# Performance work log

Measured on AMD Instinct MI355X. Metric: run time of the kernel, lower is better.

Reference implementation:

```python
import jax, jax.numpy as jnp
import numpy as np

N_EMBD = 1024
N_HEAD = 16
HEAD_DIM = N_EMBD // N_HEAD


def setup_inputs() -> dict:
    key = jax.random.key(0)
    kx, kq, kk, kv, kp = jax.random.split(key, 5)
    B, S = 4, 2048
    x = jax.random.normal(kx, (B, S, N_EMBD), dtype=jnp.float32)
    # nn.Linear(n, n, bias=False): weight [out, in], y = x @ W.T
    s = 1.0 / np.sqrt(N_EMBD)
    Wq = jax.random.uniform(kq, (N_EMBD, N_EMBD), jnp.float32, -s, s)
    Wk = jax.random.uniform(kk, (N_EMBD, N_EMBD), jnp.float32, -s, s)
    Wv = jax.random.uniform(kv, (N_EMBD, N_EMBD), jnp.float32, -s, s)
    Wo = jax.random.uniform(kp, (N_EMBD, N_EMBD), jnp.float32, -s, s)
    return {"x": x, "Wq": Wq, "Wk": Wk, "Wv": Wv, "Wo": Wo}


def _split_heads(t):
    B, S, _ = t.shape
    return t.reshape(B, S, N_HEAD, HEAD_DIM).transpose(0, 2, 1, 3)  # [B,H,S,D]


def reference(x, Wq, Wk, Wv, Wo):
    q = _split_heads(x @ Wq.T)
    k = _split_heads(x @ Wk.T)
    v = _split_heads(x @ Wv.T)
    scale = 1.0 / np.sqrt(HEAD_DIM)
    scores = jnp.einsum('bhqd,bhkd->bhqk', q, k) * scale  # [B,H,S,S]
    S = x.shape[1]
    mask = jnp.tril(jnp.ones((S, S), dtype=bool))
    masked = jnp.where(mask[None, None], scores, -jnp.inf)
    attn = jax.nn.softmax(masked, axis=-1)
    heads = jnp.einsum('bhqk,bhkd->bhqd', attn, v)
    merged = heads.transpose(0, 2, 1, 3).reshape(x.shape[0], S, N_EMBD)
    return merged @ Wo.T
```

## Files before the change

kernel.cpp:

```cpp
#include <hip/hip_runtime.h>
#include <hip/hip_bf16.h>

typedef __hip_bfloat16 bf16;
typedef __attribute__((ext_vector_type(8))) short short8;
typedef __attribute__((ext_vector_type(4))) short short4v;
typedef __attribute__((ext_vector_type(4))) float f32x4;
typedef unsigned int uint32;

#define MFMA16(a, b, c) __builtin_amdgcn_mfma_f32_16x16x32_bf16(a, b, c, 0, 0, 0)

__device__ __forceinline__ f32x4 MFMA16K16(short4v a, short4v b, f32x4 c) {
#if __has_builtin(__builtin_amdgcn_mfma_f32_16x16x16bf16_1k)
    return __builtin_amdgcn_mfma_f32_16x16x16bf16_1k(a, b, c, 0, 0, 0);
#else
    asm("v_mfma_f32_16x16x16_bf16 %0, %1, %2, %0" : "+v"(c) : "v"(a), "v"(b));
    return c;
#endif
}

constexpr int EMB   = 1024;
constexpr int SEQ   = 2048;
constexpr int BATCH = 4;
constexpr int NH    = 16;
constexpr int HD    = 64;
constexpr int QKVW  = 3 * EMB;
constexpr float QSCALE = 0.125f * 1.44269504f;

__device__ __forceinline__ void gl_lds16(const bf16* g, bf16* l) {
    __builtin_amdgcn_global_load_lds(
        (const __attribute__((address_space(1))) void*)g,
        (__attribute__((address_space(3))) void*)l,
        16, 0, 0);
}

__device__ __forceinline__ float fexp2(float x) {
#if __has_builtin(__builtin_amdgcn_exp2f)
    return __builtin_amdgcn_exp2f(x);
#else
    return exp2f(x);
#endif
}

__device__ __forceinline__ uint32 pack2(float a, float b) {
    uint32 ua = __builtin_bit_cast(uint32, a) + 0x8000u;
    uint32 ub = __builtin_bit_cast(uint32, b) + 0x8000u;
    return __builtin_amdgcn_perm(ub, ua, 0x07060302u);
}

__device__ __forceinline__ bf16 fbf16(float f) {
    unsigned short u =
        (unsigned short)((__builtin_bit_cast(uint32, f) + 0x8000u) >> 16);
    return __builtin_bit_cast(bf16, u);
}

__global__ void convert_all(const float* __restrict__ x,
                            const float* __restrict__ wq,
                            const float* __restrict__ wk,
                            const float* __restrict__ wv,
                            const float* __restrict__ wo,
                            bf16* __restrict__ xc,
                            bf16* __restrict__ wqkv,
                            bf16* __restrict__ woc) {
    const int NX = BATCH * SEQ * EMB;
    const int NW = EMB * EMB;
    const float* src; bf16* dst; int n4, b0, nb;
    const int blk = blockIdx.x;
    if (blk < 2048)      { src = x;  dst = xc;          n4 = NX / 4; b0 = 0;    nb = 2048; }
    else if (blk < 2304) { src = wq; dst = wqkv;        n4 = NW / 4; b0 = 2048; nb = 256; }
    else if (blk < 2560) { src = wk; dst = wqkv + NW;   n4 = NW / 4; b0 = 2304; nb = 256; }
    else if (blk < 2816) { src = wv; dst = wqkv + 2*NW; n4 = NW / 4; b0 = 2560; nb = 256; }
    else                 { src = wo; dst = woc;         n4 = NW / 4; b0 = 2816; nb = 256; }
    for (int i = (blk - b0) * 256 + threadIdx.x; i < n4; i += nb * 256) {
        float4 v = ((const float4*)src)[i];
        uint2 o;
        o.x = pack2(v.x, v.y);
        o.y = pack2(v.z, v.w);
        ((uint2*)dst)[i] = o;
    }
}

template <typename OutT>
__global__ __launch_bounds__(256) void gemm_bt(const bf16* __restrict__ A,
                                               const bf16* __restrict__ B,
                                               OutT* __restrict__ C,
                                               int M, int N, int K,
                                               float oscale, int qlim) {
    __shared__ __align__(16) bf16 As[2][128 * 64];
    __shared__ __align__(16) bf16 Bs[2][128 * 64];

    const int t    = threadIdx.x;
    const int lane = t & 63;
    const int wid  = t >> 6;
    const int l16  = lane & 15;
    const int quad = lane >> 4;
    const int e    = l16 & 7;
    const int wm   = (wid >> 1) * 64;
    const int wn   = (wid & 1) * 64;

    const int nwg   = (int)gridDim.x;
    const int cpx   = nwg >> 3;
    const int gx    = N >> 7;
    const int mrows = cpx / gx;
    const int xcd   = (int)blockIdx.x & 7;
    const int local = (int)blockIdx.x >> 3;
    const int m0    = (xcd * mrows + (local % mrows)) * 128;
    const int n0    = (local / mrows) * 128;
    const float sc  = (n0 < qlim) ? oscale : 1.0f;

    f32x4 acc[4][4] = {};
    const int srow = lane >> 3;
    const int scol = ((lane & 7) ^ srow) * 8;

    auto stage = [&](int kt, int buf) {
        const int k0 = kt * 64;
        #pragma unroll
        for (int it = 0; it < 4; ++it) {
            int rb = it * 32 + wid * 8;
            gl_lds16(&A[(size_t)(m0 + rb + srow) * K + k0 + scol], &As[buf][rb * 64]);
            gl_lds16(&B[(size_t)(n0 + rb + srow) * K + k0 + scol], &Bs[buf][rb * 64]);
        }
    };

    const int nk = K >> 6;
    stage(0, 0);
    stage(1, 1);

    for (int kt = 0; kt < nk; ++kt) {
        const int cur = kt & 1;
        if (kt < nk - 1) __builtin_amdgcn_s_waitcnt(0x0F78);
        else             __builtin_amdgcn_s_waitcnt(0x0F70);
        __builtin_amdgcn_s_barrier();

        #pragma unroll
        for (int ks = 0; ks < 64; ks += 32) {
            const int cb = (ks >> 3) + quad;
            short8 af[4], bfr[4];
            #pragma unroll
            for (int i = 0; i < 4; ++i)
                af[i] = *(const short8*)&As[cur][(wm + i * 16 + l16) * 64 + ((cb ^ e) * 8)];
            #pragma unroll
            for (int j = 0; j < 4; ++j)
                bfr[j] = *(const short8*)&Bs[cur][(wn + j * 16 + l16) * 64 + ((cb ^ e) * 8)];
            #pragma unroll
            for (int i = 0; i < 4; ++i)
                #pragma unroll
                for (int j = 0; j < 4; ++j)
                    acc[i][j] = MFMA16(af[i], bfr[j], acc[i][j]);
        }

        __builtin_amdgcn_s_barrier();
        if (kt + 2 < nk) stage(kt + 2, cur);
    }

    #pragma unroll
    for (int i = 0; i < 4; ++i)
        #pragma unroll
        for (int j = 0; j < 4; ++j)
            #pragma unroll
            for (int r = 0; r < 4; ++r) {
                int row = m0 + wm + i * 16 + quad * 4 + r;
                int col = n0 + wn + j * 16 + l16;
                float v = acc[i][j][r] * sc;
                if constexpr (sizeof(OutT) == 2)
                    C[(size_t)row * N + col] = fbf16(v);
                else
                    C[(size_t)row * N + col] = (OutT)v;
            }
}

__global__ __launch_bounds__(256) void transpose_v(const bf16* __restrict__ QKV,
                                                   bf16* __restrict__ Vt) {
    __shared__ __align__(16) bf16 Ts[4096];
    const int t  = threadIdx.x;
    const int st = blockIdx.x;
    const int bh = blockIdx.y;
    const int b  = bh >> 4, h = bh & 15;
    const int s0 = st * 64;

    const bf16* src = QKV + ((size_t)(b * SEQ + s0)) * QKVW + 2 * EMB + h * HD;
    {
        int r = t >> 3, cq = t & 7;
        #pragma unroll
        for (int it = 0; it < 2; ++it, r += 32) {
            uint4 v = *(const uint4*)&src[(size_t)r * QKVW + cq * 8];
            int blk = cq ^ (r >> 3);
            *(uint4*)&Ts[r * 64 + blk * 8] = v;
        }
    }
    __syncthreads();
    bf16* dst = Vt + (size_t)bh * HD * SEQ + s0;
    {
        int d = t >> 3;
        const int sq = t & 7;
        #pragma unroll
        for (int it = 0; it < 2; ++it, d += 32) {
            short8 ov;
            #pragma unroll
            for (int i = 0; i < 8; ++i) {
                int s = sq * 8 + i;
                ov[i] = (short)__bfloat16_as_ushort(
                    Ts[s * 64 + (((d >> 3) ^ sq) << 3) + (d & 7)]);
            }
            *(short8*)&dst[(size_t)d * SEQ + sq * 8] = ov;
        }
    }
}

__global__ __launch_bounds__(256, 2) void flash_attn(const bf16* __restrict__ QKV,
                                                     const bf16* __restrict__ Vt,
                                                     bf16* __restrict__ O) {
    __shared__ __align__(16) float smemF[16896];
    bf16* Ks  = (bf16*)smemF;
    bf16* VTs = (bf16*)smemF + 8192;
    constexpr int OF0  = 12480;
    constexpr int LRED = 16640;

    const int t    = threadIdx.x;
    const int lane = t & 63;
    const int w    = t >> 6;
    const int l16  = lane & 15;
    const int quad = lane >> 4;
    const int e    = l16 & 7;
    const int w16k = w * 16;

    const int lin = (int)blockIdx.x;
    const int wg  = ((lin & 7) << 6) + (lin >> 3);
    const int bh  = wg >> 3;
    const int g   = wg & 7;
    const int b   = bh >> 4, h = bh & 15;

    const bf16* Qp = QKV + (size_t)b * SEQ * QKVW + h * HD;
    const bf16* Kp = QKV + (size_t)b * SEQ * QKVW + EMB + h * HD;
    const bf16* Vp = Vt + (size_t)bh * HD * SEQ;
    bf16* Op = O + (size_t)b * SEQ * EMB + h * HD;

    const int srow = lane >> 3;
    const int scol = ((lane & 7) ^ srow) * 8;

    auto stage = [&](int kt, int buf) {
        const int kbase = kt * 64;
        #pragma unroll
        for (int it = 0; it < 2; ++it) {
            int rb = it * 32 + w * 8;
            gl_lds16(&Kp[(size_t)(kbase + rb + srow) * QKVW + scol], &Ks[buf * 4096 + rb * 64]);
            gl_lds16(&Vp[(size_t)(rb + srow) * SEQ + kbase + scol], &VTs[buf * 4096 + rb * 64]);
        }
    };

    for (int pass = 0; pass < 4; ++pass) {
        int qt;
        if      (pass == 0) qt = 31 - g;
        else if (pass == 1) qt = 16 + g;
        else if (pass == 2) qt = 15 - g;
        else                qt = g;
        const int q0 = qt * 64;

        short8 bQ[4][2];
        #pragma unroll
        for (int qg = 0; qg < 4; ++qg) {
            const size_t qr = (size_t)(q0 + qg * 16 + l16) * QKVW;
            bQ[qg][0] = *(const short8*)&Qp[qr + quad * 8];
            bQ[qg][1] = *(const short8*)&Qp[qr + 32 + quad * 8];
        }

        f32x4 o[4][4] = {};
        float lrow[4] = {0.f, 0.f, 0.f, 0.f};

        const int ntiles = qt + 1;

        stage(0, 0);
        if (ntiles > 1) stage(1, 1);

        for (int kt = 0; kt < ntiles; ++kt) {
            const int cur = kt & 1;
            const int kbase = kt * 64;
            if (kt < ntiles - 1) __builtin_amdgcn_s_waitcnt(0x0F74);
            else                 __builtin_amdgcn_s_waitcnt(0x0F70);
            __builtin_amdgcn_s_barrier();

            const bf16* Kb = &Ks[cur * 4096];
            const short8 kf0 = *(const short8*)&Kb[(w16k + l16) * 64 + ((quad ^ e) * 8)];
            const short8 kf1 = *(const short8*)&Kb[(w16k + l16) * 64 + (((4 + quad) ^ e) * 8)];

            short4v pb[4];
            const bool diag = (kt == ntiles - 1);
            const int kgb = kbase + w16k + quad * 4;
            #pragma unroll
            for (int qg = 0; qg < 4; ++qg) {
                f32x4 acc = {};
                acc = MFMA16(kf0, bQ[qg][0], acc);
                acc = MFMA16(kf1, bQ[qg][1], acc);
                float p0 = fexp2(acc[0]);
                float p1 = fexp2(acc[1]);
                float p2 = fexp2(acc[2]);
                float p3 = fexp2(acc[3]);
                if (diag) {
                    const int qglob = q0 + qg * 16 + l16;
                    if (kgb     > qglob) p0 = 0.f;
                    if (kgb + 1 > qglob) p1 = 0.f;
                    if (kgb + 2 > qglob) p2 = 0.f;
                    if (kgb + 3 > qglob) p3 = 0.f;
                }
                lrow[qg] += (p0 + p1) + (p2 + p3);
                uint2 u;
                u.x = pack2(p0, p1);
                u.y = pack2(p2, p3);
                pb[qg] = __builtin_bit_cast(short4v, u);
            }

            const bf16* Vb = &VTs[cur * 4096];
            #pragma unroll
            for (int dg = 0; dg < 4; ++dg) {
                const short4v vf = *(const short4v*)&Vb[(dg * 16 + l16) * 64 +
                    (((2 * w + (quad >> 1)) ^ e) * 8) + (quad & 1) * 4];
                #pragma unroll
                for (int qg = 0; qg < 4; ++qg)
                    o[dg][qg] = MFMA16K16(vf, pb[qg], o[dg][qg]);
            }

            __builtin_amdgcn_s_barrier();
            if (kt + 2 < ntiles) stage(kt + 2, cur);
        }

        #pragma unroll
        for (int qg = 0; qg < 4; ++qg) {
            float l = lrow[qg];
            l += __shfl_xor(l, 16);
            l += __shfl_xor(l, 32);
            lrow[qg] = l;
        }
        if (quad == 0) {
            #pragma unroll
            for (int qg = 0; qg < 4; ++qg)
                smemF[LRED + w * 64 + qg * 16 + l16] = lrow[qg];
        }
        #pragma unroll
        for (int dg = 0; dg < 4; ++dg) {
            if (dg == w) continue;
            const int slot = dg * 3 + (w < dg ? w : w - 1);
            float* pf = smemF + slot * 1040 + quad * 4 * 65 + l16;
            #pragma unroll
            for (int r = 0; r < 4; ++r)
                #pragma unroll
                for (int qg = 0; qg < 4; ++qg)
                    pf[r * 65 + qg * 16] = o[dg][qg][r];
        }
        __syncthreads();
        #pragma unroll
        for (int dg = 0; dg < 4; ++dg) {
            if (dg != w) continue;
            #pragma unroll
            for (int s = 0; s < 3; ++s) {
                const float* pf = smemF + (dg * 3 + s) * 1040 + quad * 4 * 65 + l16;
                #pragma unroll
                for (int r = 0; r < 4; ++r)
                    #pragma unroll
                    for (int qg = 0; qg < 4; ++qg)
                        o[dg][qg][r] += pf[r * 65 + qg * 16];
            }
            float rlq[4];
            #pragma unroll
            for (int qg = 0; qg < 4; ++qg) {
                float s0 = smemF[LRED +       qg * 16 + l16]
                         + smemF[LRED +  64 + qg * 16 + l16]
                         + smemF[LRED + 128 + qg * 16 + l16]
                         + smemF[LRED + 192 + qg * 16 + l16];
                rlq[qg] = 1.0f / s0;
            }
            float* Of = smemF + OF0 + w * 1040;
            #pragma unroll
            for (int r = 0; r < 4; ++r)
                #pragma unroll
                for (int qg = 0; qg < 4; ++qg)
                    Of[(quad * 4 + r) * 65 + qg * 16 + l16] = o[dg][qg][r] * rlq[qg];
            float f[16];
            #pragma unroll
            for (int d = 0; d < 16; ++d) f[d] = Of[d * 65 + lane];
            uint4 ua, ub;
            ua.x = pack2(f[0],  f[1]);  ua.y = pack2(f[2],  f[3]);
            ua.z = pack2(f[4],  f[5]);  ua.w = pack2(f[6],  f[7]);
            ub.x = pack2(f[8],  f[9]);  ub.y = pack2(f[10], f[11]);
            ub.z = pack2(f[12], f[13]); ub.w = pack2(f[14], f[15]);
            *(uint4*)&Op[(size_t)(q0 + lane) * EMB + w16k]     = ua;
            *(uint4*)&Op[(size_t)(q0 + lane) * EMB + w16k + 8] = ub;
        }
        __syncthreads();
    }
}

extern "C" void kernel_launch(void* const* d_in, const int* in_sizes, int n_in,
                              void* d_out, int out_size, void* d_ws, size_t ws_size,
                              hipStream_t stream) {
    const float* x  = (const float*)d_in[0];
    const float* Wq = (const float*)d_in[1];
    const float* Wk = (const float*)d_in[2];
    const float* Wv = (const float*)d_in[3];
    const float* Wo = (const float*)d_in[4];
    float* out = (float*)d_out;
    bf16*  ws  = (bf16*)d_ws;

    const int M  = BATCH * SEQ;
    const int NX = M * EMB;
    const int NW = EMB * EMB;

    bf16* xc   = ws;
    bf16* Ab   = xc;
    bf16* Wqkv = ws + (size_t)NX;
    bf16* Woc  = Wqkv + 3 * (size_t)NW;
    bf16* QKV  = Woc + NW;
    bf16* Vt   = QKV + (size_t)M * QKVW;

    convert_all<<<3072, 256, 0, stream>>>(x, Wq, Wk, Wv, Wo, xc, Wqkv, Woc);

    gemm_bt<bf16><<<dim3((QKVW / 128) * (M / 128)), 256, 0, stream>>>(
        xc, Wqkv, QKV, M, QKVW, EMB, QSCALE, EMB);

    transpose_v<<<dim3(SEQ / 64, BATCH * NH), 256, 0, stream>>>(QKV, Vt);

    flash_attn<<<dim3(512), 256, 0, stream>>>(QKV, Vt, Ab);

    gemm_bt<float><<<dim3((EMB / 128) * (M / 128)), 256, 0, stream>>>(
        Ab, Woc, out, M, EMB, EMB, 1.0f, 0);
}
```

Before: 245.9 us.

## Shrink flash-attn LDS via butterfly reduction, double grid and occupancy

The cross-wave output reduction changes from an all-to-all shared-memory exchange to a two-stage butterfly. This cuts shared memory from about 66KB to about 34KB per block, and the launch bound is raised from 2 to 4 blocks per CU. The grid doubles to 1024 blocks, each processing 2 balanced query tiles instead of 4. The cost is extra barriers in the epilogue and possible register pressure under the tighter launch bound.

Result: slower. 345.0 us (+40.3%).

```diff
diff --git a/kernel.cpp b/kernel.cpp
--- a/kernel.cpp
+++ b/kernel.cpp
@@ -206,14 +206,13 @@
     }
 }
 
-__global__ __launch_bounds__(256, 2) void flash_attn(const bf16* __restrict__ QKV,
+__global__ __launch_bounds__(256, 4) void flash_attn(const bf16* __restrict__ QKV,
                                                      const bf16* __restrict__ Vt,
                                                      bf16* __restrict__ O) {
-    __shared__ __align__(16) float smemF[16896];
+    __shared__ __align__(16) float smemF[8576];
     bf16* Ks  = (bf16*)smemF;
     bf16* VTs = (bf16*)smemF + 8192;
-    constexpr int OF0  = 12480;
-    constexpr int LRED = 16640;
+    constexpr int LRED = 8320;
 
     const int t    = threadIdx.x;
     const int lane = t & 63;
@@ -224,9 +223,9 @@
     const int w16k = w * 16;
 
     const int lin = (int)blockIdx.x;
-    const int wg  = ((lin & 7) << 6) + (lin >> 3);
-    const int bh  = wg >> 3;
-    const int g   = wg & 7;
+    const int wg  = ((lin & 7) << 7) + (lin >> 3);
+    const int bh  = wg >> 4;
+    const int pr  = wg & 15;
     const int b   = bh >> 4, h = bh & 15;
 
     const bf16* Qp = QKV + (size_t)b * SEQ * QKVW + h * HD;
@@ -247,12 +246,8 @@
         }
     };
 
-    for (int pass = 0; pass < 4; ++pass) {
-        int qt;
-        if      (pass == 0) qt = 31 - g;
-        else if (pass == 1) qt = 16 + g;
-        else if (pass == 2) qt = 15 - g;
-        else                qt = g;
+    for (int pass = 0; pass < 2; ++pass) {
+        const int qt = pass ? pr : 31 - pr;
         const int q0 = qt * 64;
 
         short8 bQ[4][2];
@@ -334,30 +329,66 @@
             for (int qg = 0; qg < 4; ++qg)
                 smemF[LRED + w * 64 + qg * 16 + l16] = lrow[qg];
         }
-        #pragma unroll
-        for (int dg = 0; dg < 4; ++dg) {
-            if (dg == w) continue;
-            const int slot = dg * 3 + (w < dg ? w : w - 1);
-            float* pf = smemF + slot * 1040 + quad * 4 * 65 + l16;
-            #pragma unroll
-            for (int r = 0; r < 4; ++r)
-                #pragma unroll
-                for (int qg = 0; qg < 4; ++qg)
-                    pf[r * 65 + qg * 16] = o[dg][qg][r];
+        {
+            float* s1a = smemF + (w * 2 + 0) * 1040;
+            float* s1b = smemF + (w * 2 + 1) * 1040;
+            #pragma unroll
+            for (int dg = 0; dg < 4; ++dg) {
+                if (dg == (w ^ 1)) {
+                    #pragma unroll
+                    for (int r = 0; r < 4; ++r)
+                        #pragma unroll
+                        for (int qg = 0; qg < 4; ++qg)
+                            s1a[(quad * 4 + r) * 65 + qg * 16 + l16] = o[dg][qg][r];
+                }
+                if (dg == (w ^ 3)) {
+                    #pragma unroll
+                    for (int r = 0; r < 4; ++r)
+                        #pragma unroll
+                        for (int qg = 0; qg < 4; ++qg)
+                            s1b[(quad * 4 + r) * 65 + qg * 16 + l16] = o[dg][qg][r];
+                }
+            }
         }
         __syncthreads();
-        #pragma unroll
-        for (int dg = 0; dg < 4; ++dg) {
-            if (dg != w) continue;
-            #pragma unroll
-            for (int s = 0; s < 3; ++s) {
-                const float* pf = smemF + (dg * 3 + s) * 1040 + quad * 4 * 65 + l16;
-                #pragma unroll
-                for (int r = 0; r < 4; ++r)
-                    #pragma unroll
-                    for (int qg = 0; qg < 4; ++qg)
-                        o[dg][qg][r] += pf[r * 65 + qg * 16];
-            }
+        {
+            const float* r1a = smemF + ((w ^ 1) * 2 + 0) * 1040;
+            const float* r1b = smemF + ((w ^ 1) * 2 + 1) * 1040;
+            #pragma unroll
+            for (int dg = 0; dg < 4; ++dg) {
+                if (dg == w) {
+                    #pragma unroll
+                    for (int r = 0; r < 4; ++r)
+                        #pragma unroll
+                        for (int qg = 0; qg < 4; ++qg)
+                            o[dg][qg][r] += r1a[(quad * 4 + r) * 65 + qg * 16 + l16];
+                }
+                if (dg == (w ^ 2)) {
+                    #pragma unroll
+                    for (int r = 0; r < 4; ++r)
+                        #pragma unroll
+                        for (int qg = 0; qg < 4; ++qg)
+                            o[dg][qg][r] += r1b[(quad * 4 + r) * 65 + qg * 16 + l16];
+                }
+            }
+        }
+        __syncthreads();
+        {
+            float* s2 = smemF + (w * 2 + 0) * 1040;
+            #pragma unroll
+            for (int dg = 0; dg < 4; ++dg) {
+                if (dg == (w ^ 2)) {
+                    #pragma unroll
+                    for (int r = 0; r < 4; ++r)
+                        #pragma unroll
+                        for (int qg = 0; qg < 4; ++qg)
+                            s2[(quad * 4 + r) * 65 + qg * 16 + l16] = o[dg][qg][r];
+                }
+            }
+        }
+        __syncthreads();
+        {
+            const float* r2 = smemF + ((w ^ 2) * 2 + 0) * 1040;
             float rlq[4];
             #pragma unroll
             for (int qg = 0; qg < 4; ++qg) {
@@ -367,12 +398,19 @@
                          + smemF[LRED + 192 + qg * 16 + l16];
                 rlq[qg] = 1.0f / s0;
             }
-            float* Of = smemF + OF0 + w * 1040;
-            #pragma unroll
-            for (int r = 0; r < 4; ++r)
-                #pragma unroll
-                for (int qg = 0; qg < 4; ++qg)
-                    Of[(quad * 4 + r) * 65 + qg * 16 + l16] = o[dg][qg][r] * rlq[qg];
+            float* Of = smemF + (w * 2 + 1) * 1040;
+            #pragma unroll
+            for (int dg = 0; dg < 4; ++dg) {
+                if (dg == w) {
+                    #pragma unroll
+                    for (int r = 0; r < 4; ++r)
+                        #pragma unroll
+                        for (int qg = 0; qg < 4; ++qg)
+                            Of[(quad * 4 + r) * 65 + qg * 16 + l16] =
+                                (o[dg][qg][r] +
+                                 r2[(quad * 4 + r) * 65 + qg * 16 + l16]) * rlq[qg];
+                }
+            }
             float f[16];
             #pragma unroll
             for (int d = 0; d < 16; ++d) f[d] = Of[d * 65 + lane];
@@ -417,7 +455,7 @@
 
     transpose_v<<<dim3(SEQ / 64, BATCH * NH), 256, 0, stream>>>(QKV, Vt);
 
-    flash_attn<<<dim3(512), 256, 0, stream>>>(QKV, Vt, Ab);
+    flash_attn<<<dim3(1024), 256, 0, stream>>>(QKV, Vt, Ab);
 
     gemm_bt<float><<<dim3((EMB / 128) * (M / 128)), 256, 0, stream>>>(
         Ab, Woc, out, M, EMB, EMB, 1.0f, 0);
```
